# Optimization experiments

Hardware: AMD Instinct MI355X
Metric: run time of the kernel (lower is better)

The kernel has to match this reference:

```python
import jax, jax.numpy as jnp
import numpy as np

B, T, H, TGT = 1024, 672, 128, 96

def _lstm_cell(x, h, c, Wih, Whh, b):
    # PyTorch gate order: i, f, g, o
    z = x @ Wih.T + h @ Whh.T + b
    i, f, g, o = jnp.split(z, 4, axis=-1)
    c = jax.nn.sigmoid(f) * c + jax.nn.sigmoid(i) * jnp.tanh(g)
    h = jax.nn.sigmoid(o) * jnp.tanh(c)
    return h, c

def _run_layer(xs, Wih, Whh, b):
    # xs: [T, B, in] time-major. Returns ys [T,B,H], final (h, c).
    B_ = xs.shape[1]
    h0 = jnp.zeros((B_, Whh.shape[1]), xs.dtype)
    def step(carry, x):
        h, c = carry
        h, c = _lstm_cell(x, h, c, Wih, Whh, b)
        return (h, c), h
    (h, c), ys = jax.lax.scan(step, (h0, h0), xs)
    return ys, h, c

def setup_inputs() -> dict:
    key = jax.random.key(0)
    ks = jax.random.split(key, 24)
    s = 1.0 / np.sqrt(H)
    u = lambda k, shape: jax.random.uniform(k, shape, jnp.float32, -s, s)
    inp = {"features": jax.random.normal(ks[0], (B, T, 1), jnp.float32)}
    # encoder layer 0 (input 1), layer 1 (input H); decoder same (decoder input is 1)
    inp["enc_Wih0"] = u(ks[1], (4 * H, 1));  inp["enc_Whh0"] = u(ks[2], (4 * H, H))
    inp["enc_b0"]   = u(ks[3], (4 * H,))
    inp["enc_Wih1"] = u(ks[4], (4 * H, H)); inp["enc_Whh1"] = u(ks[5], (4 * H, H))
    inp["enc_b1"]   = u(ks[6], (4 * H,))
    inp["dec_Wih0"] = u(ks[7], (4 * H, 1));  inp["dec_Whh0"] = u(ks[8], (4 * H, H))
    inp["dec_b0"]   = u(ks[9], (4 * H,))
    inp["dec_Wih1"] = u(ks[10], (4 * H, H)); inp["dec_Whh1"] = u(ks[11], (4 * H, H))
    inp["dec_b1"]   = u(ks[12], (4 * H,))
    inp["W_out1"] = u(ks[13], (H, H)); inp["b_out1"] = u(ks[14], (H,))
    inp["W_out2"] = u(ks[15], (1, H)); inp["b_out2"] = u(ks[16], (1,))
    return inp

def reference(features, enc_Wih0, enc_Whh0, enc_b0, enc_Wih1, enc_Whh1, enc_b1,
              dec_Wih0, dec_Whh0, dec_b0, dec_Wih1, dec_Whh1, dec_b1,
              W_out1, b_out1, W_out2, b_out2):
    xs = jnp.transpose(features, (1, 0, 2))  # [T, B, 1]
    ys0, h1, c1 = _run_layer(xs, enc_Wih0, enc_Whh0, enc_b0)
    _,   h2, c2 = _run_layer(ys0, enc_Wih1, enc_Whh1, enc_b1)
    x0 = jnp.zeros((features.shape[0], 1), features.dtype)
    def dec_step(carry, _):
        h1, c1, h2, c2, x = carry
        h1, c1 = _lstm_cell(x, h1, c1, dec_Wih0, dec_Whh0, dec_b0)
        h2, c2 = _lstm_cell(h1, h2, c2, dec_Wih1, dec_Whh1, dec_b1)
        pred = jax.nn.relu(h2 @ W_out1.T + b_out1) @ W_out2.T + b_out2  # [B,1]
        return (h1, c1, h2, c2, pred), pred
    _, preds = jax.lax.scan(dec_step, (h1, c1, h2, c2, x0), None, length=TGT)
    return jnp.transpose(preds[:, :, 0], (1, 0))  # [B, TGT]
```

## Files before the change

### kernel.cpp

```cpp
#include <hip/hip_runtime.h>


#define B_    1024
#define T_    672
#define H_    128
#define G_    512
#define TGT_  96
#define NBLK_ 256

typedef __attribute__((ext_vector_type(8))) short  short8;
typedef __attribute__((ext_vector_type(4))) float  floatx4;

__device__ __forceinline__ float sigm(float x)   { return 1.f / (1.f + __expf(-x)); }
__device__ __forceinline__ float tanh_f(float x) { return 1.f - 2.f / (1.f + __expf(2.f * x)); }

__device__ __forceinline__ void bsplit(float a, unsigned short& h, unsigned short& l) {
    const unsigned int u  = __float_as_uint(a);
    const unsigned int hi = (u + 0x8000u) >> 16;
    const float fh = __uint_as_float(hi << 16);
    h = (unsigned short)hi;
    l = (unsigned short)(__float_as_uint(a - fh) >> 16);
}

struct PrepArgs {
    const float* dwhh0; float* pk0;
    const float* d1x; const float* d1h; float* pack;
    const float* bsrc[3];
    unsigned short* bh[3];
    unsigned short* bl[3];
};

__global__ void kPrep(PrepArgs a) {
    const int m = blockIdx.x;
    if (m == 0) {
        for (int i = threadIdx.x; i < H_ * H_; i += blockDim.x) {
            const int k = i >> 7, j4 = i & 127;
            float* p = a.pk0 + ((size_t)k * H_ + j4) * 4;
#pragma unroll
            for (int g = 0; g < 4; g++)
                p[g] = a.dwhh0[(j4 + 128 * g) * H_ + k];
        }
    } else if (m == 1) {
        for (int i = threadIdx.x; i < H_ * H_; i += blockDim.x) {
            const int k = i >> 7, j4 = i & 127;
            float* p = a.pack + ((size_t)k * H_ + j4) * 8;
#pragma unroll
            for (int g = 0; g < 4; g++) {
                p[g]     = a.d1x[(j4 + 128 * g) * H_ + k];
                p[4 + g] = a.d1h[(j4 + 128 * g) * H_ + k];
            }
        }
    } else {
        const int s = m - 2;
        const float* src = a.bsrc[s];
        unsigned short* dh = a.bh[s];
        unsigned short* dl = a.bl[s];
        for (int i = threadIdx.x; i < G_ * H_; i += blockDim.x) {
            unsigned short h, l;
            bsplit(src[i], h, l);
            dh[i] = h; dl[i] = l;
        }
    }
}

__device__ __forceinline__ void runL0(
    const float* __restrict__ feat,
    const unsigned short* __restrict__ WHh,
    const unsigned short* __restrict__ WHl,
    const float* __restrict__ wih0,
    const float* __restrict__ bias,
    unsigned short* __restrict__ Ah,
    unsigned short* __restrict__ Al,
    float* __restrict__ hS, float* __restrict__ cS,
    int t0, int CL, int bidx,
    unsigned short (*hh)[16][136], unsigned short (*hl)[16][136], float* fsh)
{
    const int tid  = threadIdx.x;
    const int lane = tid & 63;
    const int w    = tid >> 6;
    const int c15  = lane & 15;
    const int q    = lane >> 4;
    const int BG   = bidx * 16;

    short8 wh[4][4], wl[4][4];
#pragma unroll
    for (int g = 0; g < 4; g++)
#pragma unroll
        for (int kt = 0; kt < 4; kt++) {
            const size_t off = (size_t)(16 * w + 128 * g + c15) * H_ + 32 * kt + 8 * q;
            wh[g][kt] = *(const short8*)(WHh + off);
            wl[g][kt] = *(const short8*)(WHl + off);
        }

    float bz[4], wx[4];
#pragma unroll
    for (int g = 0; g < 4; g++) {
        bz[g] = bias[16 * w + 128 * g + c15];
        wx[g] = wih0[16 * w + 128 * g + c15];
    }

    for (int i = tid; i < CL * 16; i += 512)
        fsh[i] = feat[(BG + (i & 15)) * T_ + t0 + (i >> 4)];

    float cc[4], hv[4];
#pragma unroll
    for (int r = 0; r < 4; r++) { cc[r] = 0.f; hv[r] = 0.f; }
    if (t0 != 0) {
#pragma unroll
        for (int r = 0; r < 4; r++) {
            const size_t si = (size_t)(BG + 4 * q + r) * H_ + 16 * w + c15;
            cc[r] = cS[si]; hv[r] = hS[si];
        }
    }
#pragma unroll
    for (int r = 0; r < 4; r++) {
        unsigned short hi, lo; bsplit(hv[r], hi, lo);
        hh[0][4 * q + r][16 * w + c15] = hi;
        hl[0][4 * q + r][16 * w + c15] = lo;
    }
    __syncthreads();

    int pb = 0;
    unsigned int hp[4];

    for (int dt = 0; dt < CL; dt++) {
        if (dt > 0) {
#pragma unroll
            for (int r = 0; r < 4; r++) {
                const size_t ai = ((size_t)(dt - 1) * B_ + BG + 4 * q + r) * H_ + 16 * w + c15;
                Ah[ai] = (unsigned short)(hp[r] & 0xffffu);
                Al[ai] = (unsigned short)(hp[r] >> 16);
            }
        }

        floatx4 acc[4];
#pragma unroll
        for (int g = 0; g < 4; g++) acc[g] = (floatx4){0.f, 0.f, 0.f, 0.f};

#pragma unroll
        for (int kt = 0; kt < 4; kt++) {
            const short8 ahv = *(const short8*)&hh[pb][c15][32 * kt + 8 * q];
            const short8 alv = *(const short8*)&hl[pb][c15][32 * kt + 8 * q];
#pragma unroll
            for (int g = 0; g < 4; g++) {
                acc[g] = __builtin_amdgcn_mfma_f32_16x16x32_bf16(ahv, wh[g][kt], acc[g], 0, 0, 0);
                acc[g] = __builtin_amdgcn_mfma_f32_16x16x32_bf16(ahv, wl[g][kt], acc[g], 0, 0, 0);
                acc[g] = __builtin_amdgcn_mfma_f32_16x16x32_bf16(alv, wh[g][kt], acc[g], 0, 0, 0);
            }
        }

        const int nb = pb ^ 1;
#pragma unroll
        for (int r = 0; r < 4; r++) {
            const float x = fsh[dt * 16 + 4 * q + r];
            const float zi = acc[0][r] + __fmaf_rn(wx[0], x, bz[0]);
            const float zf = acc[1][r] + __fmaf_rn(wx[1], x, bz[1]);
            const float zg = acc[2][r] + __fmaf_rn(wx[2], x, bz[2]);
            const float zo = acc[3][r] + __fmaf_rn(wx[3], x, bz[3]);
            cc[r] = sigm(zf) * cc[r] + sigm(zi) * tanh_f(zg);
            const float h = sigm(zo) * tanh_f(cc[r]);
            hv[r] = h;
            unsigned short hi, lo; bsplit(h, hi, lo);
            hp[r] = (unsigned int)hi | ((unsigned int)lo << 16);
            hh[nb][4 * q + r][16 * w + c15] = hi;
            hl[nb][4 * q + r][16 * w + c15] = lo;
        }
        __syncthreads();
        pb = nb;
    }

#pragma unroll
    for (int r = 0; r < 4; r++) {
        const size_t ai = ((size_t)(CL - 1) * B_ + BG + 4 * q + r) * H_ + 16 * w + c15;
        Ah[ai] = (unsigned short)(hp[r] & 0xffffu);
        Al[ai] = (unsigned short)(hp[r] >> 16);
        const size_t si = (size_t)(BG + 4 * q + r) * H_ + 16 * w + c15;
        hS[si] = hv[r]; cS[si] = cc[r];
    }
}

__device__ __forceinline__ void runL1(
    const float* __restrict__ X1,
    const unsigned short* __restrict__ WHh,
    const unsigned short* __restrict__ WHl,
    float* __restrict__ hS, float* __restrict__ cS,
    int t0, int CL, int bidx,
    unsigned short (*hh)[16][136], unsigned short (*hl)[16][136])
{
    const int tid  = threadIdx.x;
    const int lane = tid & 63;
    const int w    = tid >> 6;
    const int c15  = lane & 15;
    const int q    = lane >> 4;
    const int BG   = bidx * 16;

    short8 wh[4][4], wl[4][4];
#pragma unroll
    for (int g = 0; g < 4; g++)
#pragma unroll
        for (int kt = 0; kt < 4; kt++) {
            const size_t off = (size_t)(16 * w + 128 * g + c15) * H_ + 32 * kt + 8 * q;
            wh[g][kt] = *(const short8*)(WHh + off);
            wl[g][kt] = *(const short8*)(WHl + off);
        }

    float cc[4], hv[4];
#pragma unroll
    for (int r = 0; r < 4; r++) { cc[r] = 0.f; hv[r] = 0.f; }
    if (t0 != 0) {
#pragma unroll
        for (int r = 0; r < 4; r++) {
            const size_t si = (size_t)(BG + 4 * q + r) * H_ + 16 * w + c15;
            cc[r] = cS[si]; hv[r] = hS[si];
        }
    }
#pragma unroll
    for (int r = 0; r < 4; r++) {
        unsigned short hi, lo; bsplit(hv[r], hi, lo);
        hh[0][4 * q + r][16 * w + c15] = hi;
        hl[0][4 * q + r][16 * w + c15] = lo;
    }
    __syncthreads();

    int pb = 0;

    for (int dt = 0; dt < CL; dt++) {
        float x1v[4][4];
#pragma unroll
        for (int g = 0; g < 4; g++)
#pragma unroll
            for (int r = 0; r < 4; r++)
                x1v[g][r] = X1[((size_t)dt * B_ + BG + 4 * q + r) * G_ + 16 * w + 128 * g + c15];

        floatx4 acc[4];
#pragma unroll
        for (int g = 0; g < 4; g++) acc[g] = (floatx4){0.f, 0.f, 0.f, 0.f};

#pragma unroll
        for (int kt = 0; kt < 4; kt++) {
            const short8 ahv = *(const short8*)&hh[pb][c15][32 * kt + 8 * q];
            const short8 alv = *(const short8*)&hl[pb][c15][32 * kt + 8 * q];
#pragma unroll
            for (int g = 0; g < 4; g++) {
                acc[g] = __builtin_amdgcn_mfma_f32_16x16x32_bf16(ahv, wh[g][kt], acc[g], 0, 0, 0);
                acc[g] = __builtin_amdgcn_mfma_f32_16x16x32_bf16(ahv, wl[g][kt], acc[g], 0, 0, 0);
                acc[g] = __builtin_amdgcn_mfma_f32_16x16x32_bf16(alv, wh[g][kt], acc[g], 0, 0, 0);
            }
        }

        const int nb = pb ^ 1;
#pragma unroll
        for (int r = 0; r < 4; r++) {
            const float zi = acc[0][r] + x1v[0][r];
            const float zf = acc[1][r] + x1v[1][r];
            const float zg = acc[2][r] + x1v[2][r];
            const float zo = acc[3][r] + x1v[3][r];
            cc[r] = sigm(zf) * cc[r] + sigm(zi) * tanh_f(zg);
            const float h = sigm(zo) * tanh_f(cc[r]);
            hv[r] = h;
            unsigned short hi, lo; bsplit(h, hi, lo);
            hh[nb][4 * q + r][16 * w + c15] = hi;
            hl[nb][4 * q + r][16 * w + c15] = lo;
        }
        __syncthreads();
        pb = nb;
    }

#pragma unroll
    for (int r = 0; r < 4; r++) {
        const size_t si = (size_t)(BG + 4 * q + r) * H_ + 16 * w + c15;
        hS[si] = hv[r]; cS[si] = cc[r];
    }
}

__global__ __launch_bounds__(512, 2) void kF(
    const float* __restrict__ feat,
    const unsigned short* __restrict__ H0h, const unsigned short* __restrict__ H0l,
    const float* __restrict__ wih0, const float* __restrict__ bias0,
    unsigned short* __restrict__ Ah, unsigned short* __restrict__ Al,
    float* __restrict__ h1S, float* __restrict__ c1S,
    const float* __restrict__ X1,
    const unsigned short* __restrict__ H1h, const unsigned short* __restrict__ H1l,
    float* __restrict__ h2S, float* __restrict__ c2S,
    int c, int CL, int NC)
{
    __shared__ __align__(16) unsigned short hh[2][16][136];
    __shared__ __align__(16) unsigned short hl[2][16][136];
    __shared__ __align__(16) float fsh[672];

    if (blockIdx.x < 64) {
        if (c < NC)
            runL0(feat, H0h, H0l, wih0, bias0, Ah, Al, h1S, c1S,
                  c * CL, CL, blockIdx.x, hh, hl, fsh);
    } else {
        if (c > 0)
            runL1(X1, H1h, H1l, h2S, c2S,
                  (c - 1) * CL, CL, blockIdx.x - 64, hh, hl);
    }
}

__global__ __launch_bounds__(256, 2) void kXm(
    const unsigned short* __restrict__ Ah,
    const unsigned short* __restrict__ Al,
    const unsigned short* __restrict__ Wh,
    const unsigned short* __restrict__ Wl,
    const float* __restrict__ bias,
    float* __restrict__ X1)
{
    __shared__ __align__(16) unsigned short Bh[128 * 128];
    __shared__ __align__(16) unsigned short Bl[128 * 128];

    const int tid = threadIdx.x;
    const int n0  = blockIdx.y * 128;

    for (int c = tid; c < 2048; c += 256) {
        const int n  = c >> 4;
        const int kb = (c & 15) << 4;
        const int sb = n * 256 + (kb ^ ((n & 7) << 4));
        *(float4*)((char*)Bh + sb) =
            *(const float4*)((const char*)Wh + (size_t)(n0 + n) * 256 + kb);
        *(float4*)((char*)Bl + sb) =
            *(const float4*)((const char*)Wl + (size_t)(n0 + n) * 256 + kb);
    }
    __syncthreads();

    const int lane = tid & 63;
    const int w    = tid >> 6;
    const int l15  = lane & 15;
    const int lq   = lane >> 4;
    const int dt   = blockIdx.z;
    const int m0   = blockIdx.x * 128 + w * 32;

    const size_t arow = ((size_t)dt * B_ + m0 + l15) * H_;
    const unsigned short* a0h = Ah + arow;
    const unsigned short* a0l = Al + arow;

    floatx4 acc[2][8];
#pragma unroll
    for (int i = 0; i < 2; i++)
#pragma unroll
        for (int j = 0; j < 8; j++)
            acc[i][j] = (floatx4){0.f, 0.f, 0.f, 0.f};

#pragma unroll
    for (int ks = 0; ks < 4; ks++) {
        const int kk = ks * 32 + 8 * lq;
        const short8 ah0 = *(const short8*)(a0h + kk);
        const short8 al0 = *(const short8*)(a0l + kk);
        const short8 ah1 = *(const short8*)(a0h + 16 * H_ + kk);
        const short8 al1 = *(const short8*)(a0l + 16 * H_ + kk);
        const int kbb = kk * 2;
#pragma unroll
        for (int nt = 0; nt < 8; nt++) {
            const int row = nt * 16 + l15;
            const int sb  = row * 256 + (kbb ^ ((row & 7) << 4));
            const short8 bh = *(const short8*)((const char*)Bh + sb);
            const short8 bl = *(const short8*)((const char*)Bl + sb);
            acc[0][nt] = __builtin_amdgcn_mfma_f32_16x16x32_bf16(ah0, bh, acc[0][nt], 0, 0, 0);
            acc[1][nt] = __builtin_amdgcn_mfma_f32_16x16x32_bf16(ah1, bh, acc[1][nt], 0, 0, 0);
            acc[0][nt] = __builtin_amdgcn_mfma_f32_16x16x32_bf16(ah0, bl, acc[0][nt], 0, 0, 0);
            acc[1][nt] = __builtin_amdgcn_mfma_f32_16x16x32_bf16(ah1, bl, acc[1][nt], 0, 0, 0);
            acc[0][nt] = __builtin_amdgcn_mfma_f32_16x16x32_bf16(al0, bh, acc[0][nt], 0, 0, 0);
            acc[1][nt] = __builtin_amdgcn_mfma_f32_16x16x32_bf16(al1, bh, acc[1][nt], 0, 0, 0);
        }
    }

#pragma unroll
    for (int nt = 0; nt < 8; nt++) {
        const float bv = bias[n0 + nt * 16 + l15];
#pragma unroll
        for (int mt = 0; mt < 2; mt++) {
            const size_t orow =
                ((size_t)dt * B_ + m0 + mt * 16 + lq * 4) * G_ + n0 + nt * 16 + l15;
#pragma unroll
            for (int r = 0; r < 4; r++)
                X1[orow + (size_t)r * G_] = acc[mt][nt][r] + bv;
        }
    }
}

__global__ __launch_bounds__(512, 2) void kD(
    const float* __restrict__ h1S, const float* __restrict__ c1S,
    const float* __restrict__ h2S, const float* __restrict__ c2S,
    const float* __restrict__ whh0P,
    const float* __restrict__ wih0,
    const float* __restrict__ b0,
    const float* __restrict__ packD1,
    const float* __restrict__ b1,
    const float* __restrict__ wo1,
    const float* __restrict__ bo1,
    const float* __restrict__ wo2,
    const float* __restrict__ bo2,
    float* __restrict__ out)
{
    __shared__ __align__(16) float h1_sh[H_ * 4];
    __shared__ __align__(16) float h2_sh[H_ * 4];
    __shared__ __align__(16) float h2t[4][H_];
    __shared__ __align__(16) float zp[4 * 2048];
    __shared__ __align__(16) float wo1s[H_ * 132];
    __shared__ float rp[8];

    const int tid = threadIdx.x;
    const int hid = tid & 127;
    const int bb  = tid >> 7;
    const int B0  = blockIdx.x * 4;

    const float b0i = b0[hid],        b0f = b0[hid + 128];
    const float b0g = b0[hid + 256],  b0o = b0[hid + 384];
    const float wxi = wih0[hid],      wxf = wih0[hid + 128];
    const float wxg = wih0[hid + 256], wxo = wih0[hid + 384];
    const float b1i = b1[hid],        b1f = b1[hid + 128];
    const float b1g = b1[hid + 256],  b1o = b1[hid + 384];

    for (int t = tid; t < H_ * 32; t += 512) {
        const int r = t >> 5, q = t & 31;
        *(float4*)&wo1s[r * 132 + q * 4] = *(const float4*)&wo1[r * H_ + q * 4];
    }

    const float wo2v = wo2[hid];
    const float bo1j = bo1[hid];
    const float bo2v = bo2[0];

    float c1 = c1S[(B0 + bb) * H_ + hid];
    float c2 = c2S[(B0 + bb) * H_ + hid];
    h1_sh[hid * 4 + bb] = h1S[(B0 + bb) * H_ + hid];
    {
        const float h2v = h2S[(B0 + bb) * H_ + hid];
        h2_sh[hid * 4 + bb] = h2v;
        h2t[bb][hid] = h2v;
    }
    if (tid < 8) rp[tid] = -0.5f * bo2v;
    __syncthreads();

    const float* hb1 = h1_sh + bb * 128;
    const float* hb2 = h2_sh + bb * 128;
    const float* pk  = packD1 + ((size_t)bb * 32 * H_ + hid) * 8;
    const float* pw0 = whh0P + (size_t)bb * 32 * 512 + hid * 4;

    for (int s = 0; s < TGT_; s++) {
        {
            float a[4][4] = {};
#pragma unroll 8
            for (int k = 0; k < 32; k++) {
                const float4 wv = *(const float4*)&pw0[(size_t)k * 512];
                const float4 h4 = *(const float4*)&hb1[k * 4];
                a[0][0] = __fmaf_rn(h4.x, wv.x, a[0][0]);
                a[0][1] = __fmaf_rn(h4.y, wv.x, a[0][1]);
                a[0][2] = __fmaf_rn(h4.z, wv.x, a[0][2]);
                a[0][3] = __fmaf_rn(h4.w, wv.x, a[0][3]);
                a[1][0] = __fmaf_rn(h4.x, wv.y, a[1][0]);
                a[1][1] = __fmaf_rn(h4.y, wv.y, a[1][1]);
                a[1][2] = __fmaf_rn(h4.z, wv.y, a[1][2]);
                a[1][3] = __fmaf_rn(h4.w, wv.y, a[1][3]);
                a[2][0] = __fmaf_rn(h4.x, wv.z, a[2][0]);
                a[2][1] = __fmaf_rn(h4.y, wv.z, a[2][1]);
                a[2][2] = __fmaf_rn(h4.z, wv.z, a[2][2]);
                a[2][3] = __fmaf_rn(h4.w, wv.z, a[2][3]);
                a[3][0] = __fmaf_rn(h4.x, wv.w, a[3][0]);
                a[3][1] = __fmaf_rn(h4.y, wv.w, a[3][1]);
                a[3][2] = __fmaf_rn(h4.z, wv.w, a[3][2]);
                a[3][3] = __fmaf_rn(h4.w, wv.w, a[3][3]);
            }
#pragma unroll
            for (int g = 0; g < 4; g++)
#pragma unroll
                for (int b = 0; b < 4; b++)
                    zp[bb * 2048 + b * 512 + hid + 128 * g] = a[g][b];
        }
        {
            float hacc = bo1j;
#pragma unroll
            for (int q = 0; q < 32; q++) {
                const float4 hq = *(const float4*)&h2t[bb][q * 4];
                const float4 wq = *(const float4*)&wo1s[hid * 132 + q * 4];
                hacc = __fmaf_rn(hq.x, wq.x, hacc);
                hacc = __fmaf_rn(hq.y, wq.y, hacc);
                hacc = __fmaf_rn(hq.z, wq.z, hacc);
                hacc = __fmaf_rn(hq.w, wq.w, hacc);
            }
            float p = fmaxf(hacc, 0.f) * wo2v;
            p += __shfl_down(p, 32); p += __shfl_down(p, 16); p += __shfl_down(p, 8);
            p += __shfl_down(p, 4);  p += __shfl_down(p, 2);  p += __shfl_down(p, 1);
            if ((tid & 63) == 0) rp[tid >> 6] = p;
        }
        __syncthreads();

        {
            const float pred = rp[2 * bb] + rp[2 * bb + 1] + bo2v;
            if (hid == 0 && s > 0) out[(B0 + bb) * TGT_ + (s - 1)] = pred;
            const int base = bb * 512 + hid;
            float zi = __fmaf_rn(wxi, pred, b0i);
            float zf = __fmaf_rn(wxf, pred, b0f);
            float zg = __fmaf_rn(wxg, pred, b0g);
            float zo = __fmaf_rn(wxo, pred, b0o);
#pragma unroll
            for (int q = 0; q < 4; q++) {
                zi += zp[q * 2048 + base];
                zf += zp[q * 2048 + base + 128];
                zg += zp[q * 2048 + base + 256];
                zo += zp[q * 2048 + base + 384];
            }
            c1 = sigm(zf) * c1 + sigm(zi) * tanh_f(zg);
            h1_sh[hid * 4 + bb] = sigm(zo) * tanh_f(c1);
        }
        __syncthreads();

        {
            float d[4][4] = {};
#pragma unroll 8
            for (int k = 0; k < 32; k++) {
                const float4 wi = *(const float4*)&pk[(size_t)k * 1024];
                const float4 wh = *(const float4*)&pk[(size_t)k * 1024 + 4];
                const float4 p1 = *(const float4*)&hb1[k * 4];
                const float4 p2 = *(const float4*)&hb2[k * 4];
                d[0][0] = __fmaf_rn(p1.x, wi.x, __fmaf_rn(p2.x, wh.x, d[0][0]));
                d[0][1] = __fmaf_rn(p1.y, wi.x, __fmaf_rn(p2.y, wh.x, d[0][1]));
                d[0][2] = __fmaf_rn(p1.z, wi.x, __fmaf_rn(p2.z, wh.x, d[0][2]));
                d[0][3] = __fmaf_rn(p1.w, wi.x, __fmaf_rn(p2.w, wh.x, d[0][3]));
                d[1][0] = __fmaf_rn(p1.x, wi.y, __fmaf_rn(p2.x, wh.y, d[1][0]));
                d[1][1] = __fmaf_rn(p1.y, wi.y, __fmaf_rn(p2.y, wh.y, d[1][1]));
                d[1][2] = __fmaf_rn(p1.z, wi.y, __fmaf_rn(p2.z, wh.y, d[1][2]));
                d[1][3] = __fmaf_rn(p1.w, wi.y, __fmaf_rn(p2.w, wh.y, d[1][3]));
                d[2][0] = __fmaf_rn(p1.x, wi.z, __fmaf_rn(p2.x, wh.z, d[2][0]));
                d[2][1] = __fmaf_rn(p1.y, wi.z, __fmaf_rn(p2.y, wh.z, d[2][1]));
                d[2][2] = __fmaf_rn(p1.z, wi.z, __fmaf_rn(p2.z, wh.z, d[2][2]));
                d[2][3] = __fmaf_rn(p1.w, wi.z, __fmaf_rn(p2.w, wh.z, d[2][3]));
                d[3][0] = __fmaf_rn(p1.x, wi.w, __fmaf_rn(p2.x, wh.w, d[3][0]));
                d[3][1] = __fmaf_rn(p1.y, wi.w, __fmaf_rn(p2.y, wh.w, d[3][1]));
                d[3][2] = __fmaf_rn(p1.z, wi.w, __fmaf_rn(p2.z, wh.w, d[3][2]));
                d[3][3] = __fmaf_rn(p1.w, wi.w, __fmaf_rn(p2.w, wh.w, d[3][3]));
            }
#pragma unroll
            for (int g = 0; g < 4; g++)
#pragma unroll
                for (int b = 0; b < 4; b++)
                    zp[bb * 2048 + b * 512 + hid + 128 * g] = d[g][b];
        }
        __syncthreads();

        {
            const int base = bb * 512 + hid;
            float zi = b1i, zf = b1f, zg = b1g, zo = b1o;
#pragma unroll
            for (int q = 0; q < 4; q++) {
                zi += zp[q * 2048 + base];
                zf += zp[q * 2048 + base + 128];
                zg += zp[q * 2048 + base + 256];
                zo += zp[q * 2048 + base + 384];
            }
            c2 = sigm(zf) * c2 + sigm(zi) * tanh_f(zg);
            const float h2v = sigm(zo) * tanh_f(c2);
            h2_sh[hid * 4 + bb] = h2v;
            h2t[bb][hid] = h2v;
        }
        __syncthreads();
    }

    {
        float hacc = bo1j;
#pragma unroll
        for (int q = 0; q < 32; q++) {
            const float4 hq = *(const float4*)&h2t[bb][q * 4];
            const float4 wq = *(const float4*)&wo1s[hid * 132 + q * 4];
            hacc = __fmaf_rn(hq.x, wq.x, hacc);
            hacc = __fmaf_rn(hq.y, wq.y, hacc);
            hacc = __fmaf_rn(hq.z, wq.z, hacc);
            hacc = __fmaf_rn(hq.w, wq.w, hacc);
        }
        float p = fmaxf(hacc, 0.f) * wo2v;
        p += __shfl_down(p, 32); p += __shfl_down(p, 16); p += __shfl_down(p, 8);
        p += __shfl_down(p, 4);  p += __shfl_down(p, 2);  p += __shfl_down(p, 1);
        if ((tid & 63) == 0) rp[tid >> 6] = p;
    }
    __syncthreads();
    if (tid < 4)
        out[(B0 + tid) * TGT_ + (TGT_ - 1)] = rp[2 * tid] + rp[2 * tid + 1] + bo2v;
}

extern "C" void kernel_launch(void* const* d_in, const int* in_sizes, int n_in,
                              void* d_out, int out_size, void* d_ws, size_t ws_size,
                              hipStream_t stream) {
    const float* feat  = (const float*)d_in[0];
    const float* eWih0 = (const float*)d_in[1];
    const float* eWhh0 = (const float*)d_in[2];
    const float* eB0   = (const float*)d_in[3];
    const float* eWih1 = (const float*)d_in[4];
    const float* eWhh1 = (const float*)d_in[5];
    const float* eB1   = (const float*)d_in[6];
    const float* dWih0 = (const float*)d_in[7];
    const float* dWhh0 = (const float*)d_in[8];
    const float* dB0   = (const float*)d_in[9];
    const float* dWih1 = (const float*)d_in[10];
    const float* dWhh1 = (const float*)d_in[11];
    const float* dB1   = (const float*)d_in[12];
    const float* Wo1   = (const float*)d_in[13];
    const float* bo1   = (const float*)d_in[14];
    const float* Wo2   = (const float*)d_in[15];
    const float* bo2   = (const float*)d_in[16];

    const size_t SZ_BH = (size_t)B_ * H_;
    const size_t SZ_W  = (size_t)G_ * H_;
    const size_t fixed_f = 4 * SZ_BH + 6 * SZ_W + 64;

    static const int cands[] = {42, 32, 28, 24, 21, 16, 14, 12, 8, 7, 6, 4, 3, 2, 1};
    int CL = 1;
    for (int ci = 0; ci < 15; ci++) {
        const size_t need = (fixed_f + (size_t)cands[ci] * B_ * (H_ + G_)) * 4;
        if (need <= ws_size) { CL = cands[ci]; break; }
    }
    const int NC = T_ / CL;

    float* ws = (float*)d_ws;
    unsigned short* Ah = (unsigned short*)ws;
    unsigned short* Al = Ah + (size_t)CL * B_ * H_;
    float* X1    = ws + (size_t)CL * B_ * H_;
    float* h1S   = X1 + (size_t)CL * B_ * G_;
    float* c1S   = h1S + SZ_BH;
    float* h2S   = c1S + SZ_BH;
    float* c2S   = h2S + SZ_BH;
    float* pk0   = c2S + SZ_BH;
    float* wtD1p = pk0 + SZ_W;
    unsigned short* Wh  = (unsigned short*)(wtD1p + 2 * SZ_W);
    unsigned short* Wl  = Wh + SZ_W;
    unsigned short* H0h = Wl + SZ_W;
    unsigned short* H0l = H0h + SZ_W;
    unsigned short* H1h = H0l + SZ_W;
    unsigned short* H1l = H1h + SZ_W;

    PrepArgs pa;
    pa.dwhh0 = dWhh0; pa.pk0 = pk0;
    pa.d1x = dWih1; pa.d1h = dWhh1; pa.pack = wtD1p;
    pa.bsrc[0] = eWih1; pa.bh[0] = Wh;  pa.bl[0] = Wl;
    pa.bsrc[1] = eWhh0; pa.bh[1] = H0h; pa.bl[1] = H0l;
    pa.bsrc[2] = eWhh1; pa.bh[2] = H1h; pa.bl[2] = H1l;
    kPrep<<<5, 256, 0, stream>>>(pa);

    for (int c = 0; c <= NC; c++) {
        kF<<<128, 512, 0, stream>>>(feat, H0h, H0l, eWih0, eB0, Ah, Al, h1S, c1S,
                                    X1, H1h, H1l, h2S, c2S, c, CL, NC);
        if (c < NC)
            kXm<<<dim3(8, 4, CL), 256, 0, stream>>>(Ah, Al, Wh, Wl, eB1, X1);
    }
    kD<<<NBLK_, 512, 0, stream>>>(h1S, c1S, h2S, c2S,
                                  pk0, dWih0, dB0,
                                  wtD1p, dB1,
                                  Wo1, bo1, Wo2, bo2,
                                  (float*)d_out);
}
```

Measured before the change: 3.287 ms.

## Fuse input-projection GEMM into the layer kernel as a three-stage software pipeline

Layer-1 input projection GEMM moves from its own kernel into the main per-chunk kernel, so layer-0 recurrence, the GEMM and layer-1 recurrence run as three concurrent stages on different chunks. Ah/Al and X1 buffers are double-buffered so adjacent stages do not conflict. This halves kernel launches and overlaps the GEMM with both recurrences. In exchange it uses more LDS per block (64KB extra for weight tiles, possibly lowering occupancy), launches 256 blocks, and doubles workspace needs, which may force a smaller chunk length.

```diff
diff --git a/kernel.cpp b/kernel.cpp
--- a/kernel.cpp
+++ b/kernel.cpp
@@ -273,47 +273,22 @@
     }
 }
 
-__global__ __launch_bounds__(512, 2) void kF(
-    const float* __restrict__ feat,
-    const unsigned short* __restrict__ H0h, const unsigned short* __restrict__ H0l,
-    const float* __restrict__ wih0, const float* __restrict__ bias0,
-    unsigned short* __restrict__ Ah, unsigned short* __restrict__ Al,
-    float* __restrict__ h1S, float* __restrict__ c1S,
-    const float* __restrict__ X1,
-    const unsigned short* __restrict__ H1h, const unsigned short* __restrict__ H1l,
-    float* __restrict__ h2S, float* __restrict__ c2S,
-    int c, int CL, int NC)
-{
-    __shared__ __align__(16) unsigned short hh[2][16][136];
-    __shared__ __align__(16) unsigned short hl[2][16][136];
-    __shared__ __align__(16) float fsh[672];
-
-    if (blockIdx.x < 64) {
-        if (c < NC)
-            runL0(feat, H0h, H0l, wih0, bias0, Ah, Al, h1S, c1S,
-                  c * CL, CL, blockIdx.x, hh, hl, fsh);
-    } else {
-        if (c > 0)
-            runL1(X1, H1h, H1l, h2S, c2S,
-                  (c - 1) * CL, CL, blockIdx.x - 64, hh, hl);
-    }
-}
-
-__global__ __launch_bounds__(256, 2) void kXm(
+__device__ __forceinline__ void runGemm(
     const unsigned short* __restrict__ Ah,
     const unsigned short* __restrict__ Al,
     const unsigned short* __restrict__ Wh,
     const unsigned short* __restrict__ Wl,
     const float* __restrict__ bias,
-    float* __restrict__ X1)
+    float* __restrict__ X1,
+    int CL, int gbid,
+    unsigned short* Bh, unsigned short* Bl)
 {
-    __shared__ __align__(16) unsigned short Bh[128 * 128];
-    __shared__ __align__(16) unsigned short Bl[128 * 128];
-
     const int tid = threadIdx.x;
-    const int n0  = blockIdx.y * 128;
-
-    for (int c = tid; c < 2048; c += 256) {
+    const int xy  = gbid & 31;
+    const int m0b = (xy >> 2) * 128;
+    const int n0  = (xy & 3) * 128;
+
+    for (int c = tid; c < 2048; c += 512) {
         const int n  = c >> 4;
         const int kb = (c & 15) << 4;
         const int sb = n * 256 + (kb ^ ((n & 7) << 4));
@@ -328,53 +303,89 @@
     const int w    = tid >> 6;
     const int l15  = lane & 15;
     const int lq   = lane >> 4;
-    const int dt   = blockIdx.z;
-    const int m0   = blockIdx.x * 128 + w * 32;
-
-    const size_t arow = ((size_t)dt * B_ + m0 + l15) * H_;
-    const unsigned short* a0h = Ah + arow;
-    const unsigned short* a0l = Al + arow;
-
-    floatx4 acc[2][8];
-#pragma unroll
-    for (int i = 0; i < 2; i++)
-#pragma unroll
-        for (int j = 0; j < 8; j++)
-            acc[i][j] = (floatx4){0.f, 0.f, 0.f, 0.f};
-
-#pragma unroll
-    for (int ks = 0; ks < 4; ks++) {
-        const int kk = ks * 32 + 8 * lq;
-        const short8 ah0 = *(const short8*)(a0h + kk);
-        const short8 al0 = *(const short8*)(a0l + kk);
-        const short8 ah1 = *(const short8*)(a0h + 16 * H_ + kk);
-        const short8 al1 = *(const short8*)(a0l + 16 * H_ + kk);
-        const int kbb = kk * 2;
+    const int m0   = m0b + w * 16;
+
+    for (int dt = gbid >> 5; dt < CL; dt += 4) {
+        const size_t arow = ((size_t)dt * B_ + m0 + l15) * H_;
+        const unsigned short* a0h = Ah + arow;
+        const unsigned short* a0l = Al + arow;
+
+        floatx4 acc[8];
+#pragma unroll
+        for (int j = 0; j < 8; j++) acc[j] = (floatx4){0.f, 0.f, 0.f, 0.f};
+
+#pragma unroll
+        for (int ks = 0; ks < 4; ks++) {
+            const int kk = ks * 32 + 8 * lq;
+            const short8 ah = *(const short8*)(a0h + kk);
+            const short8 al = *(const short8*)(a0l + kk);
+            const int kbb = kk * 2;
+#pragma unroll
+            for (int nt = 0; nt < 8; nt++) {
+                const int row = nt * 16 + l15;
+                const int sb  = row * 256 + (kbb ^ ((row & 7) << 4));
+                const short8 bh = *(const short8*)((const char*)Bh + sb);
+                const short8 bl = *(const short8*)((const char*)Bl + sb);
+                acc[nt] = __builtin_amdgcn_mfma_f32_16x16x32_bf16(ah, bh, acc[nt], 0, 0, 0);
+                acc[nt] = __builtin_amdgcn_mfma_f32_16x16x32_bf16(ah, bl, acc[nt], 0, 0, 0);
+                acc[nt] = __builtin_amdgcn_mfma_f32_16x16x32_bf16(al, bh, acc[nt], 0, 0, 0);
+            }
+        }
+
 #pragma unroll
         for (int nt = 0; nt < 8; nt++) {
-            const int row = nt * 16 + l15;
-            const int sb  = row * 256 + (kbb ^ ((row & 7) << 4));
-            const short8 bh = *(const short8*)((const char*)Bh + sb);
-            const short8 bl = *(const short8*)((const char*)Bl + sb);
-            acc[0][nt] = __builtin_amdgcn_mfma_f32_16x16x32_bf16(ah0, bh, acc[0][nt], 0, 0, 0);
-            acc[1][nt] = __builtin_amdgcn_mfma_f32_16x16x32_bf16(ah1, bh, acc[1][nt], 0, 0, 0);
-            acc[0][nt] = __builtin_amdgcn_mfma_f32_16x16x32_bf16(ah0, bl, acc[0][nt], 0, 0, 0);
-            acc[1][nt] = __builtin_amdgcn_mfma_f32_16x16x32_bf16(ah1, bl, acc[1][nt], 0, 0, 0);
-            acc[0][nt] = __builtin_amdgcn_mfma_f32_16x16x32_bf16(al0, bh, acc[0][nt], 0, 0, 0);
-            acc[1][nt] = __builtin_amdgcn_mfma_f32_16x16x32_bf16(al1, bh, acc[1][nt], 0, 0, 0);
-        }
-    }
-
-#pragma unroll
-    for (int nt = 0; nt < 8; nt++) {
-        const float bv = bias[n0 + nt * 16 + l15];
-#pragma unroll
-        for (int mt = 0; mt < 2; mt++) {
-            const size_t orow =
-                ((size_t)dt * B_ + m0 + mt * 16 + lq * 4) * G_ + n0 + nt * 16 + l15;
+            const float bv = bias[n0 + nt * 16 + l15];
+            const size_t orow = ((size_t)dt * B_ + m0 + lq * 4) * G_ + n0 + nt * 16 + l15;
 #pragma unroll
             for (int r = 0; r < 4; r++)
-                X1[orow + (size_t)r * G_] = acc[mt][nt][r] + bv;
+                X1[orow + (size_t)r * G_] = acc[nt][r] + bv;
+        }
+    }
+}
+
+struct KFArgs {
+    const float* feat;
+    const unsigned short *H0h, *H0l;
+    const float *wih0, *bias0;
+    unsigned short *Ah0, *Al0, *Ah1, *Al1;
+    float *h1S, *c1S;
+    const unsigned short *Wh, *Wl;
+    const float* bias1;
+    float *X1a, *X1b;
+    const unsigned short *H1h, *H1l;
+    float *h2S, *c2S;
+    int c, CL, NC;
+};
+
+__global__ __launch_bounds__(512, 2) void kF(KFArgs a) {
+    __shared__ __align__(16) unsigned short hh[2][16][136];
+    __shared__ __align__(16) unsigned short hl[2][16][136];
+    __shared__ __align__(16) float fsh[672];
+    __shared__ __align__(16) unsigned short Bh[128 * 128];
+    __shared__ __align__(16) unsigned short Bl[128 * 128];
+
+    const int c = a.c;
+    if (blockIdx.x < 64) {
+        if (c < a.NC) {
+            unsigned short* Ah = (c & 1) ? a.Ah1 : a.Ah0;
+            unsigned short* Al = (c & 1) ? a.Al1 : a.Al0;
+            runL0(a.feat, a.H0h, a.H0l, a.wih0, a.bias0, Ah, Al, a.h1S, a.c1S,
+                  c * a.CL, a.CL, blockIdx.x, hh, hl, fsh);
+        }
+    } else if (blockIdx.x < 192) {
+        if (c >= 1 && c <= a.NC) {
+            const int g = c - 1;
+            const unsigned short* Ah = (g & 1) ? a.Ah1 : a.Ah0;
+            const unsigned short* Al = (g & 1) ? a.Al1 : a.Al0;
+            float* X1 = (g & 1) ? a.X1b : a.X1a;
+            runGemm(Ah, Al, a.Wh, a.Wl, a.bias1, X1, a.CL, blockIdx.x - 64, Bh, Bl);
+        }
+    } else {
+        if (c >= 2) {
+            const int l = c - 2;
+            const float* X1 = (l & 1) ? a.X1b : a.X1a;
+            runL1(X1, a.H1h, a.H1l, a.h2S, a.c2S, l * a.CL, a.CL,
+                  blockIdx.x - 192, hh, hl);
         }
     }
 }
@@ -605,16 +616,19 @@
     static const int cands[] = {42, 32, 28, 24, 21, 16, 14, 12, 8, 7, 6, 4, 3, 2, 1};
     int CL = 1;
     for (int ci = 0; ci < 15; ci++) {
-        const size_t need = (fixed_f + (size_t)cands[ci] * B_ * (H_ + G_)) * 4;
+        const size_t need = (fixed_f + 2 * (size_t)cands[ci] * B_ * (H_ + G_)) * 4;
         if (need <= ws_size) { CL = cands[ci]; break; }
     }
     const int NC = T_ / CL;
 
     float* ws = (float*)d_ws;
-    unsigned short* Ah = (unsigned short*)ws;
-    unsigned short* Al = Ah + (size_t)CL * B_ * H_;
-    float* X1    = ws + (size_t)CL * B_ * H_;
-    float* h1S   = X1 + (size_t)CL * B_ * G_;
+    unsigned short* Ah0 = (unsigned short*)ws;
+    unsigned short* Al0 = Ah0 + (size_t)CL * B_ * H_;
+    unsigned short* Ah1 = Al0 + (size_t)CL * B_ * H_;
+    unsigned short* Al1 = Ah1 + (size_t)CL * B_ * H_;
+    float* X1a   = ws + 2 * (size_t)CL * B_ * H_;
+    float* X1b   = X1a + (size_t)CL * B_ * G_;
+    float* h1S   = X1b + (size_t)CL * B_ * G_;
     float* c1S   = h1S + SZ_BH;
     float* h2S   = c1S + SZ_BH;
     float* c2S   = h2S + SZ_BH;
@@ -635,11 +649,18 @@
     pa.bsrc[2] = eWhh1; pa.bh[2] = H1h; pa.bl[2] = H1l;
     kPrep<<<5, 256, 0, stream>>>(pa);
 
-    for (int c = 0; c <= NC; c++) {
-        kF<<<128, 512, 0, stream>>>(feat, H0h, H0l, eWih0, eB0, Ah, Al, h1S, c1S,
-                                    X1, H1h, H1l, h2S, c2S, c, CL, NC);
-        if (c < NC)
-            kXm<<<dim3(8, 4, CL), 256, 0, stream>>>(Ah, Al, Wh, Wl, eB1, X1);
+    KFArgs fa;
+    fa.feat = feat; fa.H0h = H0h; fa.H0l = H0l; fa.wih0 = eWih0; fa.bias0 = eB0;
+    fa.Ah0 = Ah0; fa.Al0 = Al0; fa.Ah1 = Ah1; fa.Al1 = Al1;
+    fa.h1S = h1S; fa.c1S = c1S;
+    fa.Wh = Wh; fa.Wl = Wl; fa.bias1 = eB1;
+    fa.X1a = X1a; fa.X1b = X1b;
+    fa.H1h = H1h; fa.H1l = H1l; fa.h2S = h2S; fa.c2S = c2S;
+    fa.CL = CL; fa.NC = NC;
+
+    for (int c = 0; c <= NC + 1; c++) {
+        fa.c = c;
+        kF<<<256, 512, 0, stream>>>(fa);
     }
     kD<<<NBLK_, 512, 0, stream>>>(h1S, c1S, h2S, c2S,
                                   pk0, dWih0, dB0,
```

New measurement: 2.837 ms. 1.16x faster.
